# Kernel optimization log

Hardware: AMD Instinct MI355X
Metric: run time of the kernel (lower is better)

Reference implementation:

```python
import jax, jax.numpy as jnp
import numpy as np

D, H, E = 1024, 4096, 8


def setup_inputs() -> dict:
    key = jax.random.key(0)
    ks = jax.random.split(key, 5)
    x = jax.random.normal(ks[0], (4, 2048, D), dtype=jnp.float32)
    gate_w = jax.random.normal(ks[1], (D, E), dtype=jnp.float32) * 0.02
    gate_b = jnp.zeros((E,), dtype=jnp.float32)
    w1 = jax.random.normal(ks[2], (E, D, H), dtype=jnp.float32) * 0.02
    b1 = jnp.zeros((E, H), dtype=jnp.float32)
    w2 = jax.random.normal(ks[3], (E, H, D), dtype=jnp.float32) * 0.02
    b2 = jnp.zeros((E, D), dtype=jnp.float32)
    return {"x": x, "gate_w": gate_w, "gate_b": gate_b,
            "w1": w1, "b1": b1, "w2": w2, "b2": b2, "top_k": 2}


def reference(x, gate_w, gate_b, w1, b1, w2, b2, top_k):
    orig_shape = x.shape
    xt = x.reshape(-1, x.shape[-1])                 # [T, D]
    logits = xt @ gate_w + gate_b                   # [T, E]
    probs = jax.nn.softmax(logits, axis=-1)
    topk_v, topk_i = jax.lax.top_k(probs, top_k)    # [T, k]
    T, n_exp = probs.shape
    # dense combine weights: zero for non-selected experts (same math as
    # sorted dispatch + weighted scatter-add in the original)
    comb = jnp.zeros((T, n_exp), xt.dtype).at[
        jnp.arange(T)[:, None], topk_i].set(topk_v)  # [T, E]

    def step(acc, params):
        W1, B1, W2, B2, g = params                  # g: [T]
        h = jax.nn.gelu(xt @ W1 + B1, approximate=False)  # exact erf GELU
        return acc + g[:, None] * (h @ W2 + B2), None

    out, _ = jax.lax.scan(step, jnp.zeros_like(xt),
                          (w1, b1, w2, b2, comb.T))
    return out.reshape(orig_shape)
```

## Files before the change

### kernel.cpp

```cpp
#include <hip/hip_runtime.h>
#include <hip/hip_bf16.h>


#define T_TOK 8192
#define DDIM  1024
#define HDIM  4096
#define NEXP  8

typedef __attribute__((ext_vector_type(8))) short sv8;
typedef __attribute__((ext_vector_type(4))) float fv4;

__device__ __forceinline__ float gelu_erf(float v) {
    return 0.5f * v * (1.0f + erff(v * 0.70710678118654752f));
}

__device__ __forceinline__ short cvt_bf16(float f) {
    __hip_bfloat16 b = __float2bfloat16(f);
    unsigned short s; __builtin_memcpy(&s, &b, 2);
    return (short)s;
}

__device__ __forceinline__ void split2(float f, short& h, short& l) {
    h = cvt_bf16(f);
    unsigned int hb = ((unsigned int)(unsigned short)h) << 16;
    float hf; __builtin_memcpy(&hf, &hb, 4);
    l = cvt_bf16(f - hf);
}

__global__ __launch_bounds__(256) void zero_kernel(float* __restrict__ out,
                                                   int n, int* __restrict__ counts) {
    int i = blockIdx.x * 256 + threadIdx.x;
    if (i < n) out[i] = 0.0f;
    if (blockIdx.x == 0 && threadIdx.x < 16) counts[threadIdx.x] = 0;
}

__global__ __launch_bounds__(256) void gate_kernel(
    const float* __restrict__ x, const float* __restrict__ gw,
    const float* __restrict__ gb, int* __restrict__ counts,
    int* __restrict__ tok_idx, float* __restrict__ tok_gate) {
    const int token = blockIdx.x * 4 + (threadIdx.x >> 6);
    const int lane  = threadIdx.x & 63;
    const float* xr = x + (size_t)token * DDIM;

    float acc[8] = {0.f, 0.f, 0.f, 0.f, 0.f, 0.f, 0.f, 0.f};
    for (int d = lane; d < DDIM; d += 64) {
        const float xv = xr[d];
        const float4 g0 = *(const float4*)(gw + d * NEXP);
        const float4 g1 = *(const float4*)(gw + d * NEXP + 4);
        acc[0] = fmaf(xv, g0.x, acc[0]); acc[1] = fmaf(xv, g0.y, acc[1]);
        acc[2] = fmaf(xv, g0.z, acc[2]); acc[3] = fmaf(xv, g0.w, acc[3]);
        acc[4] = fmaf(xv, g1.x, acc[4]); acc[5] = fmaf(xv, g1.y, acc[5]);
        acc[6] = fmaf(xv, g1.z, acc[6]); acc[7] = fmaf(xv, g1.w, acc[7]);
    }
#pragma unroll
    for (int e = 0; e < 8; ++e)
        for (int off = 32; off > 0; off >>= 1)
            acc[e] += __shfl_down(acc[e], off);

    if (lane == 0) {
#pragma unroll
        for (int e = 0; e < 8; ++e) acc[e] += gb[e];
        float m = acc[0];
#pragma unroll
        for (int e = 1; e < 8; ++e) m = fmaxf(m, acc[e]);
        float p[8], s = 0.f;
#pragma unroll
        for (int e = 0; e < 8; ++e) { p[e] = expf(acc[e] - m); s += p[e]; }
        const float inv = 1.0f / s;
#pragma unroll
        for (int e = 0; e < 8; ++e) p[e] *= inv;
        int i1 = 0;
#pragma unroll
        for (int e = 1; e < 8; ++e) if (p[e] > p[i1]) i1 = e;
        int i2 = (i1 == 0) ? 1 : 0;
#pragma unroll
        for (int e = 0; e < 8; ++e) if (e != i1 && p[e] > p[i2]) i2 = e;

        int pos1 = atomicAdd(&counts[i1], 1);
        tok_idx[i1 * T_TOK + pos1]  = token;
        tok_gate[i1 * T_TOK + pos1] = p[i1];
        int pos2 = atomicAdd(&counts[i2], 1);
        tok_idx[i2 * T_TOK + pos2]  = token;
        tok_gate[i2 * T_TOK + pos2] = p[i2];
    }
}

__global__ void offs_kernel(const int* __restrict__ counts, int* __restrict__ offs) {
    if (threadIdx.x == 0 && blockIdx.x == 0) {
        int s = 0;
#pragma unroll
        for (int e = 0; e < NEXP; ++e) { offs[e] = s; s += counts[e]; }
        offs[NEXP] = s;
    }
}

__global__ __launch_bounds__(512) void ffn1_mfma(
    const float* __restrict__ x, const float* __restrict__ w1,
    const float* __restrict__ b1, const int* __restrict__ counts,
    const int* __restrict__ offs, const int* __restrict__ tok_idx,
    unsigned short* __restrict__ Hbuf) {
    const int e   = blockIdx.z;
    const int cnt = counts[e];
    const int m0  = blockIdx.y * 256;
    if (m0 >= cnt) return;
    const int n0  = blockIdx.x * 128;

    __shared__ __align__(16) short Ah[256][40], Al[256][40];
    __shared__ __align__(16) short Bh[128][40], Bl[128][40];
    __shared__ int stok[256];

    const int tid  = threadIdx.x;
    const int lane = tid & 63;
    const int wv   = tid >> 6;
    const int wr   = wv >> 1, wc = wv & 1;
    const int r16  = lane & 15, g4 = lane >> 4;

    if (tid < 256) stok[tid] = tok_idx[e * T_TOK + min(m0 + tid, cnt - 1)];
    __syncthreads();

    const float* W = w1 + (size_t)e * DDIM * HDIM;

    fv4 acc[4][4];
    const fv4 z4 = {0.f, 0.f, 0.f, 0.f};
#pragma unroll
    for (int i = 0; i < 4; ++i)
#pragma unroll
        for (int j = 0; j < 4; ++j) acc[i][j] = z4;

    for (int k0 = 0; k0 < DDIM; k0 += 32) {
#pragma unroll
        for (int h = 0; h < 2; ++h) {
            const int c   = tid + h * 512;
            const int row = c >> 2, kc = c & 3;
            const float* src = x + (size_t)stok[row] * DDIM + k0 + kc * 8;
            const float4 f0 = *(const float4*)src;
            const float4 f1 = *(const float4*)(src + 4);
            const float f[8] = {f0.x, f0.y, f0.z, f0.w, f1.x, f1.y, f1.z, f1.w};
            sv8 hv, lv;
#pragma unroll
            for (int i = 0; i < 8; ++i) { short hh, ll; split2(f[i], hh, ll); hv[i] = hh; lv[i] = ll; }
            *(sv8*)&Ah[row][kc * 8] = hv;
            *(sv8*)&Al[row][kc * 8] = lv;
        }
        {
            const int nn = tid >> 2, kc = tid & 3;
            float f[8];
#pragma unroll
            for (int i = 0; i < 8; ++i)
                f[i] = W[(size_t)(k0 + kc * 8 + i) * HDIM + n0 + nn];
            sv8 hv, lv;
#pragma unroll
            for (int i = 0; i < 8; ++i) { short hh, ll; split2(f[i], hh, ll); hv[i] = hh; lv[i] = ll; }
            *(sv8*)&Bh[nn][kc * 8] = hv;
            *(sv8*)&Bl[nn][kc * 8] = lv;
        }
        __syncthreads();

        sv8 a_h[4], a_l[4], b_h[4], b_l[4];
#pragma unroll
        for (int m = 0; m < 4; ++m) {
            const int row = wr * 64 + m * 16 + r16;
            a_h[m] = *(const sv8*)&Ah[row][g4 * 8];
            a_l[m] = *(const sv8*)&Al[row][g4 * 8];
        }
#pragma unroll
        for (int n = 0; n < 4; ++n) {
            const int col = wc * 64 + n * 16 + r16;
            b_h[n] = *(const sv8*)&Bh[col][g4 * 8];
            b_l[n] = *(const sv8*)&Bl[col][g4 * 8];
        }
#pragma unroll
        for (int m = 0; m < 4; ++m)
#pragma unroll
            for (int n = 0; n < 4; ++n) {
                acc[m][n] = __builtin_amdgcn_mfma_f32_16x16x32_bf16(a_h[m], b_h[n], acc[m][n], 0, 0, 0);
                acc[m][n] = __builtin_amdgcn_mfma_f32_16x16x32_bf16(a_h[m], b_l[n], acc[m][n], 0, 0, 0);
                acc[m][n] = __builtin_amdgcn_mfma_f32_16x16x32_bf16(a_l[m], b_h[n], acc[m][n], 0, 0, 0);
            }
        __syncthreads();
    }

    const int hbase = offs[e] + m0;
#pragma unroll
    for (int n = 0; n < 4; ++n) {
        const int colg = n0 + wc * 64 + n * 16 + r16;
        const float bias = b1[e * HDIM + colg];
#pragma unroll
        for (int m = 0; m < 4; ++m) {
#pragma unroll
            for (int r = 0; r < 4; ++r) {
                const int rowl = wr * 64 + m * 16 + g4 * 4 + r;
                if (m0 + rowl < cnt) {
                    const float v = gelu_erf(acc[m][n][r] + bias);
                    Hbuf[(size_t)(hbase + rowl) * HDIM + colg] = (unsigned short)cvt_bf16(v);
                }
            }
        }
    }
}

__global__ __launch_bounds__(512) void ffn2_mfma(
    const unsigned short* __restrict__ Hb, const float* __restrict__ w2,
    const float* __restrict__ b2, const int* __restrict__ counts,
    const int* __restrict__ offs, const int* __restrict__ tok_idx,
    const float* __restrict__ tok_gate, float* __restrict__ out) {
    const int e   = blockIdx.z;
    const int cnt = counts[e];
    const int m0  = blockIdx.y * 256;
    if (m0 >= cnt) return;
    const int n0  = blockIdx.x * 128;

    __shared__ __align__(16) short Ahs[256][40];
    __shared__ __align__(16) short Bh[128][40], Bl[128][40];
    __shared__ int   stok[256];
    __shared__ float sgate[256];

    const int tid  = threadIdx.x;
    const int lane = tid & 63;
    const int wv   = tid >> 6;
    const int wr   = wv >> 1, wc = wv & 1;
    const int r16  = lane & 15, g4 = lane >> 4;

    if (tid < 256) {
        const int src = e * T_TOK + min(m0 + tid, cnt - 1);
        stok[tid]  = tok_idx[src];
        sgate[tid] = tok_gate[src];
    }
    __syncthreads();

    const float* W = w2 + (size_t)e * HDIM * DDIM;
    const int oe = offs[e];

    fv4 acc[4][4];
    const fv4 z4 = {0.f, 0.f, 0.f, 0.f};
#pragma unroll
    for (int i = 0; i < 4; ++i)
#pragma unroll
        for (int j = 0; j < 4; ++j) acc[i][j] = z4;

    for (int k0 = 0; k0 < HDIM; k0 += 32) {
#pragma unroll
        for (int h = 0; h < 2; ++h) {
            const int c   = tid + h * 512;
            const int row = c >> 2, kc = c & 3;
            const size_t grow = (size_t)(oe + min(m0 + row, cnt - 1));
            *(sv8*)&Ahs[row][kc * 8] = *(const sv8*)(Hb + grow * HDIM + k0 + kc * 8);
        }
        {
            const int nn = tid >> 2, kc = tid & 3;
            float f[8];
#pragma unroll
            for (int i = 0; i < 8; ++i)
                f[i] = W[(size_t)(k0 + kc * 8 + i) * DDIM + n0 + nn];
            sv8 hv, lv;
#pragma unroll
            for (int i = 0; i < 8; ++i) { short hh, ll; split2(f[i], hh, ll); hv[i] = hh; lv[i] = ll; }
            *(sv8*)&Bh[nn][kc * 8] = hv;
            *(sv8*)&Bl[nn][kc * 8] = lv;
        }
        __syncthreads();

        sv8 a[4], b_h[4], b_l[4];
#pragma unroll
        for (int m = 0; m < 4; ++m) {
            const int row = wr * 64 + m * 16 + r16;
            a[m] = *(const sv8*)&Ahs[row][g4 * 8];
        }
#pragma unroll
        for (int n = 0; n < 4; ++n) {
            const int col = wc * 64 + n * 16 + r16;
            b_h[n] = *(const sv8*)&Bh[col][g4 * 8];
            b_l[n] = *(const sv8*)&Bl[col][g4 * 8];
        }
#pragma unroll
        for (int m = 0; m < 4; ++m)
#pragma unroll
            for (int n = 0; n < 4; ++n) {
                acc[m][n] = __builtin_amdgcn_mfma_f32_16x16x32_bf16(a[m], b_h[n], acc[m][n], 0, 0, 0);
                acc[m][n] = __builtin_amdgcn_mfma_f32_16x16x32_bf16(a[m], b_l[n], acc[m][n], 0, 0, 0);
            }
        __syncthreads();
    }

#pragma unroll
    for (int n = 0; n < 4; ++n) {
        const int colg = n0 + wc * 64 + n * 16 + r16;
        const float bias = b2[e * DDIM + colg];
#pragma unroll
        for (int m = 0; m < 4; ++m) {
#pragma unroll
            for (int r = 0; r < 4; ++r) {
                const int rowl = wr * 64 + m * 16 + g4 * 4 + r;
                if (m0 + rowl < cnt) {
                    const int   t  = stok[rowl];
                    const float gg = sgate[rowl];
                    atomicAdd(&out[(size_t)t * DDIM + colg], gg * (acc[m][n][r] + bias));
                }
            }
        }
    }
}

extern "C" void kernel_launch(void* const* d_in, const int* in_sizes, int n_in,
                              void* d_out, int out_size, void* d_ws, size_t ws_size,
                              hipStream_t stream) {
    const float* x      = (const float*)d_in[0];
    const float* gate_w = (const float*)d_in[1];
    const float* gate_b = (const float*)d_in[2];
    const float* w1     = (const float*)d_in[3];
    const float* b1     = (const float*)d_in[4];
    const float* w2     = (const float*)d_in[5];
    const float* b2     = (const float*)d_in[6];

    char* ws        = (char*)d_ws;
    int*   counts   = (int*)ws;
    int*   offs     = (int*)(ws + 64);
    int*   tok_idx  = (int*)(ws + 1024);
    float* tok_gate = (float*)(ws + 1024 + 262144);
    unsigned short* Hbuf = (unsigned short*)(ws + (1 << 20));

    float* out = (float*)d_out;

    zero_kernel<<<(T_TOK * DDIM + 255) / 256, 256, 0, stream>>>(out, T_TOK * DDIM, counts);
    gate_kernel<<<T_TOK / 4, 256, 0, stream>>>(x, gate_w, gate_b, counts, tok_idx, tok_gate);
    offs_kernel<<<1, 64, 0, stream>>>(counts, offs);

    dim3 g1(HDIM / 128, T_TOK / 256, NEXP);
    dim3 g2(DDIM / 128, T_TOK / 256, NEXP);
    ffn1_mfma<<<g1, 512, 0, stream>>>(x, w1, b1, counts, offs, tok_idx, Hbuf);
    ffn2_mfma<<<g2, 512, 0, stream>>>(Hbuf, w2, b2, counts, offs, tok_idx, tok_gate, out);
}
```

Before: 1.532 ms.

## Pre-split x into bf16 hi/lo and register-prefetch next K tile in FFN GEMMs

```diff
diff --git a/kernel.cpp b/kernel.cpp
--- a/kernel.cpp
+++ b/kernel.cpp
@@ -32,6 +32,21 @@
     int i = blockIdx.x * 256 + threadIdx.x;
     if (i < n) out[i] = 0.0f;
     if (blockIdx.x == 0 && threadIdx.x < 16) counts[threadIdx.x] = 0;
+}
+
+__global__ __launch_bounds__(256) void split_x_kernel(
+    const float* __restrict__ x, unsigned short* __restrict__ xh,
+    unsigned short* __restrict__ xl) {
+    const size_t i = ((size_t)blockIdx.x * 256 + threadIdx.x) * 8;
+    if (i >= (size_t)T_TOK * DDIM) return;
+    const float4 f0 = *(const float4*)(x + i);
+    const float4 f1 = *(const float4*)(x + i + 4);
+    const float f[8] = {f0.x, f0.y, f0.z, f0.w, f1.x, f1.y, f1.z, f1.w};
+    sv8 hv, lv;
+#pragma unroll
+    for (int j = 0; j < 8; ++j) { short hh, ll; split2(f[j], hh, ll); hv[j] = hh; lv[j] = ll; }
+    *(sv8*)(xh + i) = hv;
+    *(sv8*)(xl + i) = lv;
 }
 
 __global__ __launch_bounds__(256) void gate_kernel(
@@ -94,7 +109,120 @@
     }
 }
 
-__global__ __launch_bounds__(512) void ffn1_mfma(
+__global__ __launch_bounds__(512) void ffn1_ps2(
+    const unsigned short* __restrict__ xh, const unsigned short* __restrict__ xl,
+    const float* __restrict__ w1, const float* __restrict__ b1,
+    const int* __restrict__ counts, const int* __restrict__ offs,
+    const int* __restrict__ tok_idx, unsigned short* __restrict__ Hbuf) {
+    const int e   = blockIdx.z;
+    const int cnt = counts[e];
+    const int m0  = blockIdx.y * 256;
+    if (m0 >= cnt) return;
+    const int n0  = blockIdx.x * 128;
+
+    __shared__ __align__(16) short Ah[256][40], Al[256][40];
+    __shared__ __align__(16) short Bh[128][40], Bl[128][40];
+    __shared__ int stok[256];
+
+    const int tid  = threadIdx.x;
+    const int lane = tid & 63;
+    const int wv   = tid >> 6;
+    const int wr   = wv >> 1, wc = wv & 1;
+    const int r16  = lane & 15, g4 = lane >> 4;
+
+    if (tid < 256) stok[tid] = tok_idx[e * T_TOK + min(m0 + tid, cnt - 1)];
+    __syncthreads();
+
+    const float* W = w1 + (size_t)e * DDIM * HDIM;
+
+    const int ar0 = tid >> 2, ar1 = 128 + (tid >> 2), akc = tid & 3;
+    const size_t t0 = (size_t)stok[ar0] * DDIM + akc * 8;
+    const size_t t1 = (size_t)stok[ar1] * DDIM + akc * 8;
+    const int bn = tid >> 2, bkc = tid & 3;
+
+    sv8 pah0 = *(const sv8*)(xh + t0);
+    sv8 pal0 = *(const sv8*)(xl + t0);
+    sv8 pah1 = *(const sv8*)(xh + t1);
+    sv8 pal1 = *(const sv8*)(xl + t1);
+    float pb[8];
+#pragma unroll
+    for (int i = 0; i < 8; ++i) pb[i] = W[(size_t)(bkc * 8 + i) * HDIM + n0 + bn];
+
+    fv4 acc[4][4];
+    const fv4 z4 = {0.f, 0.f, 0.f, 0.f};
+#pragma unroll
+    for (int i = 0; i < 4; ++i)
+#pragma unroll
+        for (int j = 0; j < 4; ++j) acc[i][j] = z4;
+
+    for (int k0 = 0; k0 < DDIM; k0 += 32) {
+        *(sv8*)&Ah[ar0][akc * 8] = pah0;
+        *(sv8*)&Al[ar0][akc * 8] = pal0;
+        *(sv8*)&Ah[ar1][akc * 8] = pah1;
+        *(sv8*)&Al[ar1][akc * 8] = pal1;
+        {
+            sv8 hv, lv;
+#pragma unroll
+            for (int i = 0; i < 8; ++i) { short hh, ll; split2(pb[i], hh, ll); hv[i] = hh; lv[i] = ll; }
+            *(sv8*)&Bh[bn][bkc * 8] = hv;
+            *(sv8*)&Bl[bn][bkc * 8] = lv;
+        }
+        const int k1 = k0 + 32;
+        if (k1 < DDIM) {
+            pah0 = *(const sv8*)(xh + t0 + k1);
+            pal0 = *(const sv8*)(xl + t0 + k1);
+            pah1 = *(const sv8*)(xh + t1 + k1);
+            pal1 = *(const sv8*)(xl + t1 + k1);
+#pragma unroll
+            for (int i = 0; i < 8; ++i)
+                pb[i] = W[(size_t)(k1 + bkc * 8 + i) * HDIM + n0 + bn];
+        }
+        __syncthreads();
+
+        sv8 a_h[4], a_l[4], b_h[4], b_l[4];
+#pragma unroll
+        for (int m = 0; m < 4; ++m) {
+            const int row = wr * 64 + m * 16 + r16;
+            a_h[m] = *(const sv8*)&Ah[row][g4 * 8];
+            a_l[m] = *(const sv8*)&Al[row][g4 * 8];
+        }
+#pragma unroll
+        for (int n = 0; n < 4; ++n) {
+            const int col = wc * 64 + n * 16 + r16;
+            b_h[n] = *(const sv8*)&Bh[col][g4 * 8];
+            b_l[n] = *(const sv8*)&Bl[col][g4 * 8];
+        }
+#pragma unroll
+        for (int m = 0; m < 4; ++m)
+#pragma unroll
+            for (int n = 0; n < 4; ++n) {
+                acc[m][n] = __builtin_amdgcn_mfma_f32_16x16x32_bf16(a_h[m], b_h[n], acc[m][n], 0, 0, 0);
+                acc[m][n] = __builtin_amdgcn_mfma_f32_16x16x32_bf16(a_h[m], b_l[n], acc[m][n], 0, 0, 0);
+                acc[m][n] = __builtin_amdgcn_mfma_f32_16x16x32_bf16(a_l[m], b_h[n], acc[m][n], 0, 0, 0);
+            }
+        __syncthreads();
+    }
+
+    const int hbase = offs[e] + m0;
+#pragma unroll
+    for (int n = 0; n < 4; ++n) {
+        const int colg = n0 + wc * 64 + n * 16 + r16;
+        const float bias = b1[e * HDIM + colg];
+#pragma unroll
+        for (int m = 0; m < 4; ++m) {
+#pragma unroll
+            for (int r = 0; r < 4; ++r) {
+                const int rowl = wr * 64 + m * 16 + g4 * 4 + r;
+                if (m0 + rowl < cnt) {
+                    const float v = gelu_erf(acc[m][n][r] + bias);
+                    Hbuf[(size_t)(hbase + rowl) * HDIM + colg] = (unsigned short)cvt_bf16(v);
+                }
+            }
+        }
+    }
+}
+
+__global__ __launch_bounds__(512) void ffn1_fb(
     const float* __restrict__ x, const float* __restrict__ w1,
     const float* __restrict__ b1, const int* __restrict__ counts,
     const int* __restrict__ offs, const int* __restrict__ tok_idx,
@@ -231,6 +359,17 @@
     const float* W = w2 + (size_t)e * HDIM * DDIM;
     const int oe = offs[e];
 
+    const int ar0 = tid >> 2, ar1 = 128 + (tid >> 2), akc = tid & 3;
+    const size_t g0r = (size_t)(oe + min(m0 + ar0, cnt - 1)) * HDIM + akc * 8;
+    const size_t g1r = (size_t)(oe + min(m0 + ar1, cnt - 1)) * HDIM + akc * 8;
+    const int bn = tid >> 2, bkc = tid & 3;
+
+    sv8 pa0 = *(const sv8*)(Hb + g0r);
+    sv8 pa1 = *(const sv8*)(Hb + g1r);
+    float pb[8];
+#pragma unroll
+    for (int i = 0; i < 8; ++i) pb[i] = W[(size_t)(bkc * 8 + i) * DDIM + n0 + bn];
+
     fv4 acc[4][4];
     const fv4 z4 = {0.f, 0.f, 0.f, 0.f};
 #pragma unroll
@@ -239,24 +378,22 @@
         for (int j = 0; j < 4; ++j) acc[i][j] = z4;
 
     for (int k0 = 0; k0 < HDIM; k0 += 32) {
-#pragma unroll
-        for (int h = 0; h < 2; ++h) {
-            const int c   = tid + h * 512;
-            const int row = c >> 2, kc = c & 3;
-            const size_t grow = (size_t)(oe + min(m0 + row, cnt - 1));
-            *(sv8*)&Ahs[row][kc * 8] = *(const sv8*)(Hb + grow * HDIM + k0 + kc * 8);
-        }
+        *(sv8*)&Ahs[ar0][akc * 8] = pa0;
+        *(sv8*)&Ahs[ar1][akc * 8] = pa1;
         {
-            const int nn = tid >> 2, kc = tid & 3;
-            float f[8];
+            sv8 hv, lv;
+#pragma unroll
+            for (int i = 0; i < 8; ++i) { short hh, ll; split2(pb[i], hh, ll); hv[i] = hh; lv[i] = ll; }
+            *(sv8*)&Bh[bn][bkc * 8] = hv;
+            *(sv8*)&Bl[bn][bkc * 8] = lv;
+        }
+        const int k1 = k0 + 32;
+        if (k1 < HDIM) {
+            pa0 = *(const sv8*)(Hb + g0r + k1);
+            pa1 = *(const sv8*)(Hb + g1r + k1);
 #pragma unroll
             for (int i = 0; i < 8; ++i)
-                f[i] = W[(size_t)(k0 + kc * 8 + i) * DDIM + n0 + nn];
-            sv8 hv, lv;
-#pragma unroll
-            for (int i = 0; i < 8; ++i) { short hh, ll; split2(f[i], hh, ll); hv[i] = hh; lv[i] = ll; }
-            *(sv8*)&Bh[nn][kc * 8] = hv;
-            *(sv8*)&Bl[nn][kc * 8] = lv;
+                pb[i] = W[(size_t)(k1 + bkc * 8 + i) * DDIM + n0 + bn];
         }
         __syncthreads();
 
@@ -318,6 +455,13 @@
     int*   tok_idx  = (int*)(ws + 1024);
     float* tok_gate = (float*)(ws + 1024 + 262144);
     unsigned short* Hbuf = (unsigned short*)(ws + (1 << 20));
+    const size_t hb_bytes = (size_t)2 * T_TOK * HDIM * sizeof(unsigned short);
+    unsigned short* xhi = (unsigned short*)(ws + (1 << 20) + hb_bytes);
+    unsigned short* xlo = xhi + (size_t)T_TOK * DDIM;
+
+    const size_t need_ps = (size_t)(1 << 20) + hb_bytes
+                         + (size_t)2 * T_TOK * DDIM * sizeof(unsigned short);
+    const bool presplit = ws_size >= need_ps;
 
     float* out = (float*)d_out;
 
@@ -327,6 +471,11 @@
 
     dim3 g1(HDIM / 128, T_TOK / 256, NEXP);
     dim3 g2(DDIM / 128, T_TOK / 256, NEXP);
-    ffn1_mfma<<<g1, 512, 0, stream>>>(x, w1, b1, counts, offs, tok_idx, Hbuf);
+    if (presplit) {
+        split_x_kernel<<<(T_TOK * DDIM) / (256 * 8), 256, 0, stream>>>(x, xhi, xlo);
+        ffn1_ps2<<<g1, 512, 0, stream>>>(xhi, xlo, w1, b1, counts, offs, tok_idx, Hbuf);
+    } else {
+        ffn1_fb<<<g1, 512, 0, stream>>>(x, w1, b1, counts, offs, tok_idx, Hbuf);
+    }
     ffn2_mfma<<<g2, 512, 0, stream>>>(Hbuf, w2, b2, counts, offs, tok_idx, tok_gate, out);
 }
```

After: 1.816 ms. 18.5% more time.
